# Kernel optimization log

Hardware: AMD Instinct MI355X
Metric: run time of the kernel (lower is better)

The kernel has to match this reference:

```python
import jax, jax.numpy as jnp
import numpy as np

B, S, D, R = 8, 512, 768, 128


def setup_inputs() -> dict:
    key = jax.random.key(0)
    k1, k2, k3 = jax.random.split(key, 3)
    embeddings = jax.random.normal(k1, (B, S, D), dtype=jnp.float32)
    # nn.init.uniform_(proj, -0.05, 0.05)
    proj_dist = jax.random.uniform(k2, (R, D), dtype=jnp.float32, minval=-0.05, maxval=0.05)
    proj_depth = jax.random.uniform(k3, (R, D), dtype=jnp.float32, minval=-0.05, maxval=0.05)
    return {"embeddings": embeddings, "proj_dist": proj_dist, "proj_depth": proj_depth}


def _distances(embeddings, proj):
    # (B,S,D) @ (D,R) -> (B,S,R)
    p = jnp.einsum('bsd,rd->bsr', embeddings, proj)
    # pairwise squared euclidean distances: sum_r (p_i - p_j)^2 -> (B,S,S)
    diff = p[:, :, None, :] - p[:, None, :, :]
    return jnp.sum(diff * diff, axis=-1)


def _depths(embeddings, proj):
    p = jnp.einsum('bsd,rd->bsr', embeddings, proj)
    return jnp.sum(p * p, axis=-1)  # (B,S)


def reference(embeddings, proj_dist, proj_depth):
    distances = _distances(embeddings, proj_dist)
    depths = _depths(embeddings, proj_depth)
    return (distances, depths)
```

## Files before the change

### kernel.cpp

```cpp
#include <hip/hip_runtime.h>

#define NB 8
#define NS 512
#define ND 768
#define NR 128
#define NM (NB * NS)
#define DIST_ELEMS ((size_t)NB * NS * NS)

typedef short bf16x8 __attribute__((ext_vector_type(8)));
typedef float f32x4  __attribute__((ext_vector_type(4)));

__device__ __forceinline__ unsigned short f2bf(float f) {
  return (unsigned short)((__float_as_uint(f) + 0x8000u) >> 16);
}
__device__ __forceinline__ float bf2f(unsigned short h) {
  return __uint_as_float(((unsigned int)h) << 16);
}
__device__ __forceinline__ bf16x8 pack8(float4 lo, float4 hi) {
  bf16x8 p;
  p[0] = (short)f2bf(lo.x); p[1] = (short)f2bf(lo.y);
  p[2] = (short)f2bf(lo.z); p[3] = (short)f2bf(lo.w);
  p[4] = (short)f2bf(hi.x); p[5] = (short)f2bf(hi.y);
  p[6] = (short)f2bf(hi.z); p[7] = (short)f2bf(hi.w);
  return p;
}

constexpr int KT  = 128;
constexpr int SAS = 136;

__global__ __launch_bounds__(256) void proj_kernel(
    const float* __restrict__ emb,
    const float* __restrict__ projD,
    const float* __restrict__ projP,
    unsigned short* __restrict__ P,
    float* __restrict__ nP0, float* __restrict__ nP1,
    float* __restrict__ nD0, float* __restrict__ nD1)
{
  __shared__ unsigned short sA[32][SAS];
  __shared__ unsigned short sB[64][SAS];
  __shared__ float sRed[4][32];

  const int tid = threadIdx.x;
  const int m0  = blockIdx.x * 32;
  const int ct  = blockIdx.y;
  const bool isP = (ct < 2);
  const float* proj = (isP ? projD : projP) + (size_t)((ct & 1) * 64) * ND;

  const int ar = tid >> 3, ao = tid & 7;
  const float* aPtr = emb + (size_t)(m0 + ar) * ND + ao * 8;
  const int br = tid >> 2, bo = tid & 3;
  const float* bPtr = proj + (size_t)br * ND + bo * 8;

  float4 a0, a1, a2, a3;
  float4 c0, c1, c2, c3, c4, c5, c6, c7;
  a0 = *(const float4*)(aPtr);      a1 = *(const float4*)(aPtr + 4);
  a2 = *(const float4*)(aPtr + 64); a3 = *(const float4*)(aPtr + 68);
  c0 = *(const float4*)(bPtr);      c1 = *(const float4*)(bPtr + 4);
  c2 = *(const float4*)(bPtr + 32); c3 = *(const float4*)(bPtr + 36);
  c4 = *(const float4*)(bPtr + 64); c5 = *(const float4*)(bPtr + 68);
  c6 = *(const float4*)(bPtr + 96); c7 = *(const float4*)(bPtr + 100);

  const int lane = tid & 63;
  const int w    = tid >> 6;
  const int ln   = lane & 15;
  const int q    = lane >> 4;

  f32x4 acc[2] = {};

  for (int kt = 0; kt < ND; kt += KT) {
    *(bf16x8*)(&sA[ar][ao * 8])        = pack8(a0, a1);
    *(bf16x8*)(&sA[ar][(ao + 8) * 8])  = pack8(a2, a3);
    *(bf16x8*)(&sB[br][bo * 8])        = pack8(c0, c1);
    *(bf16x8*)(&sB[br][(bo + 4) * 8])  = pack8(c2, c3);
    *(bf16x8*)(&sB[br][(bo + 8) * 8])  = pack8(c4, c5);
    *(bf16x8*)(&sB[br][(bo + 12) * 8]) = pack8(c6, c7);
    __syncthreads();
    if (kt + KT < ND) {
      const int o = kt + KT;
      a0 = *(const float4*)(aPtr + o);      a1 = *(const float4*)(aPtr + o + 4);
      a2 = *(const float4*)(aPtr + o + 64); a3 = *(const float4*)(aPtr + o + 68);
      c0 = *(const float4*)(bPtr + o);      c1 = *(const float4*)(bPtr + o + 4);
      c2 = *(const float4*)(bPtr + o + 32); c3 = *(const float4*)(bPtr + o + 36);
      c4 = *(const float4*)(bPtr + o + 64); c5 = *(const float4*)(bPtr + o + 68);
      c6 = *(const float4*)(bPtr + o + 96); c7 = *(const float4*)(bPtr + o + 100);
    }
    #pragma unroll
    for (int ks = 0; ks < 4; ++ks) {
      bf16x8 bq = *(const bf16x8*)(&sB[16 * w + ln][ks * 32 + q * 8]);
      #pragma unroll
      for (int i = 0; i < 2; ++i) {
        bf16x8 aq = *(const bf16x8*)(&sA[16 * i + ln][ks * 32 + q * 8]);
        acc[i] = __builtin_amdgcn_mfma_f32_16x16x32_bf16(aq, bq, acc[i], 0, 0, 0);
      }
    }
    __syncthreads();
  }

  const int colG = (ct & 1) * 64 + 16 * w + ln;
  #pragma unroll
  for (int i = 0; i < 2; ++i)
    #pragma unroll
    for (int r = 0; r < 4; ++r) {
      unsigned short hb = f2bf(acc[i][r]);
      if (isP) P[(size_t)(m0 + 16 * i + 4 * q + r) * NR + colG] = hb;
      float v = bf2f(hb);
      float s = v * v;
      s += __shfl_xor(s, 1);
      s += __shfl_xor(s, 2);
      s += __shfl_xor(s, 4);
      s += __shfl_xor(s, 8);
      if (ln == 0) sRed[w][16 * i + 4 * q + r] = s;
    }
  __syncthreads();
  if (tid < 32) {
    float* np = (ct == 0) ? nP0 : (ct == 1) ? nP1 : (ct == 2) ? nD0 : nD1;
    np[m0 + tid] = sRed[0][tid] + sRed[1][tid] + sRed[2][tid] + sRed[3][tid];
  }
}

__global__ __launch_bounds__(256) void dist_kernel(
    const unsigned short* __restrict__ P,
    const float* __restrict__ nP0, const float* __restrict__ nP1,
    const float* __restrict__ nD0, const float* __restrict__ nD1,
    float* __restrict__ out,
    float* __restrict__ depths)
{
  __shared__ float nIs[64], nJs[64];

  const int tid = threadIdx.x;
  const int b  = blockIdx.z;
  const int i0 = blockIdx.y * 64;
  const int j0 = blockIdx.x * 64;
  const unsigned short* Pb = P + (size_t)b * NS * NR;
  const int mB = b * NS;

  if (tid < 64) {
    nIs[tid] = nP0[mB + i0 + tid] + nP1[mB + i0 + tid];
  } else if (tid < 128) {
    const int t = tid - 64;
    nJs[t] = nP0[mB + j0 + t] + nP1[mB + j0 + t];
  } else if (blockIdx.x == 0 && tid < 192) {
    const int t = tid - 128;
    depths[mB + i0 + t] = nD0[mB + i0 + t] + nD1[mB + i0 + t];
  }

  const int lane = tid & 63;
  const int w    = tid >> 6;
  const int ln   = lane & 15;
  const int q    = lane >> 4;

  bf16x8 aq[4][4], bq[4];
  #pragma unroll
  for (int ks = 0; ks < 4; ++ks) {
    bq[ks] = *(const bf16x8*)(Pb + (size_t)(j0 + 16 * w + ln) * NR + ks * 32 + q * 8);
    #pragma unroll
    for (int i = 0; i < 4; ++i)
      aq[i][ks] = *(const bf16x8*)(Pb + (size_t)(i0 + 16 * i + ln) * NR + ks * 32 + q * 8);
  }
  __syncthreads();

  f32x4 acc[4] = {};
  #pragma unroll
  for (int ks = 0; ks < 4; ++ks)
    #pragma unroll
    for (int i = 0; i < 4; ++i)
      acc[i] = __builtin_amdgcn_mfma_f32_16x16x32_bf16(aq[i][ks], bq[ks], acc[i], 0, 0, 0);

  const int col = j0 + 16 * w + ln;
  const float nj = nJs[16 * w + ln];
  float* ob = out + (size_t)b * NS * NS;
  #pragma unroll
  for (int i = 0; i < 4; ++i)
    #pragma unroll
    for (int r = 0; r < 4; ++r) {
      const int rloc = 16 * i + 4 * q + r;
      ob[(size_t)(i0 + rloc) * NS + col] = nIs[rloc] + nj - 2.0f * acc[i][r];
    }
}

extern "C" void kernel_launch(void* const* d_in, const int* in_sizes, int n_in,
                              void* d_out, int out_size, void* d_ws, size_t ws_size,
                              hipStream_t stream) {
  const float* emb   = (const float*)d_in[0];
  const float* projD = (const float*)d_in[1];
  const float* projP = (const float*)d_in[2];
  float* out = (float*)d_out;

  unsigned short* P = (unsigned short*)d_ws;
  float* nP0 = (float*)((char*)d_ws + (size_t)NM * NR * 2);
  float* nP1 = nP0 + NM;
  float* nD0 = nP1 + NM;
  float* nD1 = nD0 + NM;
  float* depths = out + DIST_ELEMS;

  proj_kernel<<<dim3(NM / 32, 4), 256, 0, stream>>>(emb, projD, projP, P, nP0, nP1, nD0, nD1);
  dist_kernel<<<dim3(NS / 64, NS / 64, NB), 256, 0, stream>>>(P, nP0, nP1, nD0, nD1, out, depths);
}
```

Before: 79.21 us.

## Double-buffer A tile, load B fragments directly, use native bf16 conversion

The projection kernel now double-buffers the embedding tile in shared memory so each K-step needs one barrier instead of two. The projection-matrix fragments are read from global memory straight into MFMA registers, which removes the sB shared buffer and its stores. Float-to-bf16 conversion switches to the compiler's __bf16 cast, which can map to hardware convert instructions but changes the rounding from round-half-up to round-to-nearest-even. In the distance kernel the barrier moves after the MFMAs, so the global loads and matrix multiply overlap the shared-memory norm setup.

```diff
diff --git a/kernel.cpp b/kernel.cpp
--- a/kernel.cpp
+++ b/kernel.cpp
@@ -8,21 +8,22 @@
 #define DIST_ELEMS ((size_t)NB * NS * NS)
 
 typedef short bf16x8 __attribute__((ext_vector_type(8)));
+typedef __bf16 bfv8  __attribute__((ext_vector_type(8)));
 typedef float f32x4  __attribute__((ext_vector_type(4)));
 
 __device__ __forceinline__ unsigned short f2bf(float f) {
-  return (unsigned short)((__float_as_uint(f) + 0x8000u) >> 16);
+  return __builtin_bit_cast(unsigned short, (__bf16)f);
 }
 __device__ __forceinline__ float bf2f(unsigned short h) {
   return __uint_as_float(((unsigned int)h) << 16);
 }
 __device__ __forceinline__ bf16x8 pack8(float4 lo, float4 hi) {
-  bf16x8 p;
-  p[0] = (short)f2bf(lo.x); p[1] = (short)f2bf(lo.y);
-  p[2] = (short)f2bf(lo.z); p[3] = (short)f2bf(lo.w);
-  p[4] = (short)f2bf(hi.x); p[5] = (short)f2bf(hi.y);
-  p[6] = (short)f2bf(hi.z); p[7] = (short)f2bf(hi.w);
-  return p;
+  bfv8 v;
+  v[0] = (__bf16)lo.x; v[1] = (__bf16)lo.y;
+  v[2] = (__bf16)lo.z; v[3] = (__bf16)lo.w;
+  v[4] = (__bf16)hi.x; v[5] = (__bf16)hi.y;
+  v[6] = (__bf16)hi.z; v[7] = (__bf16)hi.w;
+  return __builtin_bit_cast(bf16x8, v);
 }
 
 constexpr int KT  = 128;
@@ -36,8 +37,7 @@
     float* __restrict__ nP0, float* __restrict__ nP1,
     float* __restrict__ nD0, float* __restrict__ nD1)
 {
-  __shared__ unsigned short sA[32][SAS];
-  __shared__ unsigned short sB[64][SAS];
+  __shared__ unsigned short sA[2][32][SAS];
   __shared__ float sRed[4][32];
 
   const int tid = threadIdx.x;
@@ -48,52 +48,54 @@
 
   const int ar = tid >> 3, ao = tid & 7;
   const float* aPtr = emb + (size_t)(m0 + ar) * ND + ao * 8;
-  const int br = tid >> 2, bo = tid & 3;
-  const float* bPtr = proj + (size_t)br * ND + bo * 8;
-
-  float4 a0, a1, a2, a3;
-  float4 c0, c1, c2, c3, c4, c5, c6, c7;
-  a0 = *(const float4*)(aPtr);      a1 = *(const float4*)(aPtr + 4);
-  a2 = *(const float4*)(aPtr + 64); a3 = *(const float4*)(aPtr + 68);
-  c0 = *(const float4*)(bPtr);      c1 = *(const float4*)(bPtr + 4);
-  c2 = *(const float4*)(bPtr + 32); c3 = *(const float4*)(bPtr + 36);
-  c4 = *(const float4*)(bPtr + 64); c5 = *(const float4*)(bPtr + 68);
-  c6 = *(const float4*)(bPtr + 96); c7 = *(const float4*)(bPtr + 100);
 
   const int lane = tid & 63;
   const int w    = tid >> 6;
   const int ln   = lane & 15;
   const int q    = lane >> 4;
 
+  const float* bRow = proj + (size_t)(16 * w + ln) * ND + q * 8;
+
+  float4 a0, a1, a2, a3;
+  a0 = *(const float4*)(aPtr);      a1 = *(const float4*)(aPtr + 4);
+  a2 = *(const float4*)(aPtr + 64); a3 = *(const float4*)(aPtr + 68);
+
   f32x4 acc[2] = {};
 
+  *(bf16x8*)(&sA[0][ar][ao * 8])       = pack8(a0, a1);
+  *(bf16x8*)(&sA[0][ar][(ao + 8) * 8]) = pack8(a2, a3);
+  __syncthreads();
+
+  int p = 0;
   for (int kt = 0; kt < ND; kt += KT) {
-    *(bf16x8*)(&sA[ar][ao * 8])        = pack8(a0, a1);
-    *(bf16x8*)(&sA[ar][(ao + 8) * 8])  = pack8(a2, a3);
-    *(bf16x8*)(&sB[br][bo * 8])        = pack8(c0, c1);
-    *(bf16x8*)(&sB[br][(bo + 4) * 8])  = pack8(c2, c3);
-    *(bf16x8*)(&sB[br][(bo + 8) * 8])  = pack8(c4, c5);
-    *(bf16x8*)(&sB[br][(bo + 12) * 8]) = pack8(c6, c7);
-    __syncthreads();
-    if (kt + KT < ND) {
+    const bool more = (kt + KT < ND);
+    if (more) {
       const int o = kt + KT;
       a0 = *(const float4*)(aPtr + o);      a1 = *(const float4*)(aPtr + o + 4);
       a2 = *(const float4*)(aPtr + o + 64); a3 = *(const float4*)(aPtr + o + 68);
-      c0 = *(const float4*)(bPtr + o);      c1 = *(const float4*)(bPtr + o + 4);
-      c2 = *(const float4*)(bPtr + o + 32); c3 = *(const float4*)(bPtr + o + 36);
-      c4 = *(const float4*)(bPtr + o + 64); c5 = *(const float4*)(bPtr + o + 68);
-      c6 = *(const float4*)(bPtr + o + 96); c7 = *(const float4*)(bPtr + o + 100);
-    }
+    }
+    bf16x8 bq[4];
     #pragma unroll
     for (int ks = 0; ks < 4; ++ks) {
-      bf16x8 bq = *(const bf16x8*)(&sB[16 * w + ln][ks * 32 + q * 8]);
+      const float* bp = bRow + kt + ks * 32;
+      float4 lo = *(const float4*)bp;
+      float4 hi = *(const float4*)(bp + 4);
+      bq[ks] = pack8(lo, hi);
+    }
+    #pragma unroll
+    for (int ks = 0; ks < 4; ++ks) {
       #pragma unroll
       for (int i = 0; i < 2; ++i) {
-        bf16x8 aq = *(const bf16x8*)(&sA[16 * i + ln][ks * 32 + q * 8]);
-        acc[i] = __builtin_amdgcn_mfma_f32_16x16x32_bf16(aq, bq, acc[i], 0, 0, 0);
+        bf16x8 aq = *(const bf16x8*)(&sA[p][16 * i + ln][ks * 32 + q * 8]);
+        acc[i] = __builtin_amdgcn_mfma_f32_16x16x32_bf16(aq, bq[ks], acc[i], 0, 0, 0);
       }
     }
+    if (more) {
+      *(bf16x8*)(&sA[p ^ 1][ar][ao * 8])       = pack8(a0, a1);
+      *(bf16x8*)(&sA[p ^ 1][ar][(ao + 8) * 8]) = pack8(a2, a3);
+    }
     __syncthreads();
+    p ^= 1;
   }
 
   const int colG = (ct & 1) * 64 + 16 * w + ln;
@@ -157,7 +159,6 @@
     for (int i = 0; i < 4; ++i)
       aq[i][ks] = *(const bf16x8*)(Pb + (size_t)(i0 + 16 * i + ln) * NR + ks * 32 + q * 8);
   }
-  __syncthreads();
 
   f32x4 acc[4] = {};
   #pragma unroll
@@ -165,6 +166,8 @@
     #pragma unroll
     for (int i = 0; i < 4; ++i)
       acc[i] = __builtin_amdgcn_mfma_f32_16x16x32_bf16(aq[i][ks], bq[ks], acc[i], 0, 0, 0);
+
+  __syncthreads();
 
   const int col = j0 + 16 * w + ln;
   const float nj = nJs[16 * w + ln];
```

Measured after the change: 85.48 us. 7.9% more time.
